# Performance work log

Measured on AMD Instinct MI355X. Metric: run time of the kernel, lower is better.

The kernel has to match this reference:

```python
import jax, jax.numpy as jnp
import numpy as np

B, NBANDS, NCHAN, NTIME = 32, 9, 64, 4096
M = 32
C = M * NBANDS          # 288 spectral-spatial channels
SF = 4                  # strideFactor
TLEN = 2 * SF - 1       # 7 overlapping temporal windows
E = 2                   # embed_dim
H = 2                   # num_heads (head_dim = 1)
NCLASS = 4
BN_EPS = 1e-5


def _renorm(w, maxnorm):
    # torch.renorm(p=2, dim=0): clamp L2 norm of each dim-0 slice to maxnorm
    norms = jnp.sqrt(jnp.sum(w.reshape(w.shape[0], -1) ** 2, axis=1))
    scale = jnp.minimum(1.0, maxnorm / jnp.maximum(norms, 1e-7))
    return w * scale.reshape((-1,) + (1,) * (w.ndim - 1))


def _pos_embed():
    # get_1d_sincos_pos_embed_from_grid(embed_dim=2, len=7)
    pos = np.arange(TLEN, dtype=np.float32)
    omega = 1.0 / (10000.0 ** (np.arange(E // 2, dtype=np.float32) / (E / 2.0)))
    out = pos[:, None] * omega[None, :]
    return jnp.asarray(np.concatenate([np.sin(out), np.cos(out)], axis=1), jnp.float32)  # [TLEN, E]


def setup_inputs() -> dict:
    key = jax.random.key(0)
    ks = jax.random.split(key, 10)
    s = 0.1
    return {
        "x": jax.random.uniform(ks[0], (B, NBANDS, NCHAN, NTIME), jnp.float32),
        "conv_w": jax.random.normal(ks[1], (C, 1, NCHAN, 1), jnp.float32) * s,
        "conv_b": jax.random.normal(ks[2], (C,), jnp.float32) * s,
        "bn_gamma": jnp.ones((C,), jnp.float32),
        "bn_beta": jnp.zeros((C,), jnp.float32),
        "bn_mean": jnp.zeros((C,), jnp.float32),
        "bn_var": jnp.ones((C,), jnp.float32),
        "in_proj_w": jax.random.normal(ks[3], (C, 3 * E, E), jnp.float32) * s,
        "in_proj_b": jax.random.normal(ks[4], (C, 3 * E), jnp.float32) * s,
        "out_proj_w": jax.random.normal(ks[5], (C, E, E), jnp.float32) * s,
        "out_proj_b": jax.random.normal(ks[6], (C, E), jnp.float32) * s,
        "last_w": jax.random.normal(ks[7], (NCLASS, C * TLEN * E), jnp.float32) * s,
        "last_b": jax.random.normal(ks[8], (NCLASS,), jnp.float32) * s,
    }


def _forward(x, conv_w, conv_b, bn_gamma, bn_beta, bn_mean, bn_var,
             in_proj_w, in_proj_b, out_proj_w, out_proj_b, last_w, last_b):
    # --- SCB: grouped conv (nChan,1) + BatchNorm(eval) + swish ---
    w = _renorm(conv_w, 2.0)
    y = jax.lax.conv_general_dilated(
        x, w, window_strides=(1, 1), padding='VALID',
        dimension_numbers=('NCHW', 'OIHW', 'NCHW'),
        feature_group_count=NBANDS) + conv_b[None, :, None, None]      # [B,C,1,NTIME]
    y = (y - bn_mean[None, :, None, None]) * jax.lax.rsqrt(bn_var + BN_EPS)[None, :, None, None]
    y = y * bn_gamma[None, :, None, None] + bn_beta[None, :, None, None]
    y = y * jax.nn.sigmoid(y)  # swish

    # --- overlapping temporal windows stacked on dim 2 ---
    ts = NTIME // (SF * 2)
    xs = jnp.concatenate([y[:, :, :, i * ts:(i + 2) * ts] for i in range(TLEN)], axis=2)  # [B,C,TLEN,2ts]

    # --- tempo_layer: log-var, RMS/mean shape factor ---
    var = jnp.log(jnp.clip(jnp.var(xs, axis=3, keepdims=True, ddof=1), 1e-6, 1e6))
    mean_ = jnp.mean(xs, axis=3, keepdims=True)
    x_rms = jnp.sqrt(jnp.mean(xs ** 2, axis=3, keepdims=True))
    feat = jnp.concatenate([var, x_rms / mean_], axis=3)               # [B,C,TLEN,E]

    # --- batched per-channel multihead self-attention (replaces C-way loop) ---
    yq = feat + _pos_embed()[None, None]                               # [B,C,T,E]
    qkv = jnp.einsum('bcte,cfe->bctf', yq, in_proj_w) + in_proj_b[None, :, None, :]
    q, k, v = jnp.split(qkv, 3, axis=3)
    hd = E // H
    q = q.reshape(B, C, TLEN, H, hd)
    k = k.reshape(B, C, TLEN, H, hd)
    v = v.reshape(B, C, TLEN, H, hd)
    scores = jnp.einsum('bcthd,bcshd->bchts', q, k) / jnp.sqrt(jnp.float32(hd))
    att = jax.nn.softmax(scores, axis=-1)
    o = jnp.einsum('bchts,bcshd->bcthd', att, v).reshape(B, C, TLEN, E)
    o = jnp.einsum('bcte,cfe->bctf', o, out_proj_w) + out_proj_b[None, :, None, :]

    # --- classifier with weight-norm constraint + log-softmax ---
    flat = o.reshape(B, C * TLEN * E)
    lw = _renorm(last_w, 0.5)
    logits = flat @ lw.T + last_b
    return jax.nn.log_softmax(logits, axis=1)


def reference(x, conv_w, conv_b, bn_gamma, bn_beta, bn_mean, bn_var,
              in_proj_w, in_proj_b, out_proj_w, out_proj_b, last_w, last_b):
    return _forward(x, conv_w, conv_b, bn_gamma, bn_beta, bn_mean, bn_var,
                    in_proj_w, in_proj_b, out_proj_w, out_proj_b, last_w, last_b)
```

## Files before the change

### kernel.cpp

```cpp
#include <hip/hip_runtime.h>
#include <math.h>

#define BB     32
#define NBANDS 9
#define NCHAN  64
#define NTIME  4096
#define CC     288
#define TLEN   7
#define NSEG   8
#define SEGLEN 512
#define NCLASS 4

#define WS_WF    0
#define WS_BIAS  (WS_WF + CC*NCHAN)
#define WS_S1    (WS_BIAS + CC)
#define WS_S2    (WS_S1 + BB*CC*NSEG)
#define WS_FLAT  (WS_S2 + BB*CC*NSEG)
#define WS_TOTAL (WS_FLAT + BB*CC*TLEN*2)

__global__ __launch_bounds__(64) void k0_fold(
    const float* __restrict__ cw, const float* __restrict__ cb,
    const float* __restrict__ gam, const float* __restrict__ bet,
    const float* __restrict__ mu, const float* __restrict__ var,
    float* __restrict__ Wf, float* __restrict__ biasf) {
  int c = blockIdx.x;
  int h = threadIdx.x;
  float w = cw[c * NCHAN + h];
  float sq = w * w;
#pragma unroll
  for (int off = 32; off; off >>= 1) sq += __shfl_down(sq, off, 64);
  sq = __shfl(sq, 0, 64);
  float norm = sqrtf(sq);
  float scale = fminf(1.0f, 2.0f / fmaxf(norm, 1e-7f));
  float bns = gam[c] / sqrtf(var[c] + 1e-5f);
  Wf[c * NCHAN + h] = w * scale * bns;
  if (h == 0) biasf[c] = (cb[c] - mu[c]) * bns + bet[c];
}

__global__ __launch_bounds__(256, 4) void k1_conv(
    const float* __restrict__ x, const float* __restrict__ Wf,
    const float* __restrict__ biasf,
    float* __restrict__ S1, float* __restrict__ S2) {
  int gid = blockIdx.x;
  int seg = gid & 7;
  int g = (gid >> 3) % NBANDS;
  int b = gid / (NBANDS * NSEG);
  int tid = threadIdx.x;
  const float* xp = x + (size_t)(b * NBANDS + g) * NCHAN * NTIME + seg * SEGLEN;
  const float* wbase = Wf + g * 32 * NCHAN;
  const float* bbase = biasf + g * 32;

  float acc0[32], acc1[32];
#pragma unroll
  for (int c = 0; c < 32; ++c) { acc0[c] = 0.0f; acc1[c] = 0.0f; }

#pragma unroll 1
  for (int ht = 0; ht < NCHAN; ht += 8) {
    float2 xv[8];
#pragma unroll
    for (int j = 0; j < 8; ++j)
      xv[j] = ((const float2*)(xp + (size_t)(ht + j) * NTIME))[tid];
#pragma unroll
    for (int c = 0; c < 32; ++c) {
#pragma unroll
      for (int j = 0; j < 8; ++j) {
        float w = wbase[c * NCHAN + ht + j];
        acc0[c] = fmaf(w, xv[j].x, acc0[c]);
        acc1[c] = fmaf(w, xv[j].y, acc1[c]);
      }
    }
  }

  __shared__ float part[32][4][2];
  int wave = tid >> 6;
  int lane = tid & 63;

#pragma unroll
  for (int c = 0; c < 32; ++c) {
    float bias = bbase[c];
    float da = acc0[c] + bias;
    float db = acc1[c] + bias;
    float ya = da * __builtin_amdgcn_rcpf(1.0f + __expf(-da));
    float yb = db * __builtin_amdgcn_rcpf(1.0f + __expf(-db));
    float s1 = ya + yb;
    float s2 = fmaf(ya, ya, yb * yb);
#pragma unroll
    for (int off = 32; off; off >>= 1) {
      s1 += __shfl_down(s1, off, 64);
      s2 += __shfl_down(s2, off, 64);
    }
    if (lane == 0) { part[c][wave][0] = s1; part[c][wave][1] = s2; }
  }
  __syncthreads();
  if (tid < 64) {
    int c = tid >> 1;
    int which = tid & 1;
    float v = part[c][0][which] + part[c][1][which] +
              part[c][2][which] + part[c][3][which];
    size_t o = (size_t)((b * CC) + g * 32 + c) * NSEG + seg;
    if (which == 0) S1[o] = v; else S2[o] = v;
  }
}

__global__ __launch_bounds__(256) void k2_attn(
    const float* __restrict__ S1, const float* __restrict__ S2,
    const float* __restrict__ ipw, const float* __restrict__ ipb,
    const float* __restrict__ opw, const float* __restrict__ opb,
    float* __restrict__ flat) {
  const float PSIN[TLEN] = {0.0f, 0.8414709848f, 0.9092974268f, 0.1411200081f,
                            -0.7568024953f, -0.9589242747f, -0.2794154982f};
  const float PCOS[TLEN] = {1.0f, 0.5403023059f, -0.4161468365f, -0.9899924966f,
                            -0.6536436209f, 0.2836621855f, 0.9601702867f};
  int idx = blockIdx.x * blockDim.x + threadIdx.x;
  if (idx >= BB * CC) return;
  int b = idx / CC, c = idx % CC;
  const float* s1 = S1 + (size_t)(b * CC + c) * NSEG;
  const float* s2 = S2 + (size_t)(b * CC + c) * NSEG;

  float yq[TLEN][2];
#pragma unroll
  for (int t = 0; t < TLEN; ++t) {
    float S1w = s1[t] + s1[t + 1];
    float S2w = s2[t] + s2[t + 1];
    float mean = S1w * (1.0f / 1024.0f);
    float var = (S2w - S1w * S1w * (1.0f / 1024.0f)) * (1.0f / 1023.0f);
    var = fminf(fmaxf(var, 1e-6f), 1e6f);
    float rms = sqrtf(S2w * (1.0f / 1024.0f));
    yq[t][0] = __logf(var) + PSIN[t];
    yq[t][1] = rms / mean + PCOS[t];
  }

  const float* W = ipw + c * 12;
  const float* Bp = ipb + c * 6;
  float q[TLEN][2], k[TLEN][2], v[TLEN][2];
#pragma unroll
  for (int t = 0; t < TLEN; ++t) {
#pragma unroll
    for (int f = 0; f < 6; ++f) {
      float val = W[f * 2 + 0] * yq[t][0] + W[f * 2 + 1] * yq[t][1] + Bp[f];
      if (f < 2) q[t][f] = val;
      else if (f < 4) k[t][f - 2] = val;
      else v[t][f - 4] = val;
    }
  }

  float o[TLEN][2];
#pragma unroll
  for (int h = 0; h < 2; ++h) {
#pragma unroll
    for (int t = 0; t < TLEN; ++t) {
      float sc[TLEN];
      float m = -1e30f;
#pragma unroll
      for (int s = 0; s < TLEN; ++s) {
        sc[s] = q[t][h] * k[s][h];
        m = fmaxf(m, sc[s]);
      }
      float sum = 0.0f, acc = 0.0f;
#pragma unroll
      for (int s = 0; s < TLEN; ++s) {
        float e = __expf(sc[s] - m);
        sum += e;
        acc += e * v[s][h];
      }
      o[t][h] = acc / sum;
    }
  }

  const float* Wo = opw + c * 4;
  const float* Bo = opb + c * 2;
  float* out = flat + (size_t)b * (CC * TLEN * 2) + c * (TLEN * 2);
#pragma unroll
  for (int t = 0; t < TLEN; ++t) {
    out[t * 2 + 0] = Wo[0] * o[t][0] + Wo[1] * o[t][1] + Bo[0];
    out[t * 2 + 1] = Wo[2] * o[t][0] + Wo[3] * o[t][1] + Bo[1];
  }
}

__global__ __launch_bounds__(256) void k3_cls(
    const float* __restrict__ flat, const float* __restrict__ lw,
    const float* __restrict__ lb, float* __restrict__ out) {
  const int FEAT = CC * TLEN * 2;
  int b = blockIdx.x;
  int tid = threadIdx.x;
  const float* f = flat + (size_t)b * FEAT;
  float d[NCLASS] = {0, 0, 0, 0}, n2[NCLASS] = {0, 0, 0, 0};
  for (int j = tid; j < FEAT; j += 256) {
    float fv = f[j];
#pragma unroll
    for (int n = 0; n < NCLASS; ++n) {
      float w = lw[n * FEAT + j];
      d[n] = fmaf(fv, w, d[n]);
      n2[n] = fmaf(w, w, n2[n]);
    }
  }
  __shared__ float red[4][8];
  int lane = tid & 63, wave = tid >> 6;
#pragma unroll
  for (int n = 0; n < NCLASS; ++n) {
#pragma unroll
    for (int off = 32; off; off >>= 1) {
      d[n] += __shfl_down(d[n], off, 64);
      n2[n] += __shfl_down(n2[n], off, 64);
    }
  }
  if (lane == 0) {
#pragma unroll
    for (int n = 0; n < NCLASS; ++n) {
      red[wave][n] = d[n];
      red[wave][n + 4] = n2[n];
    }
  }
  __syncthreads();
  if (tid == 0) {
    float logit[NCLASS];
#pragma unroll
    for (int n = 0; n < NCLASS; ++n) {
      float dn = red[0][n] + red[1][n] + red[2][n] + red[3][n];
      float nn = red[0][n + 4] + red[1][n + 4] + red[2][n + 4] + red[3][n + 4];
      float norm = sqrtf(nn);
      float scale = fminf(1.0f, 0.5f / fmaxf(norm, 1e-7f));
      logit[n] = dn * scale + lb[n];
    }
    float m = fmaxf(fmaxf(logit[0], logit[1]), fmaxf(logit[2], logit[3]));
    float s = 0.0f;
#pragma unroll
    for (int n = 0; n < NCLASS; ++n) s += expf(logit[n] - m);
    float ls = logf(s);
#pragma unroll
    for (int n = 0; n < NCLASS; ++n) out[b * NCLASS + n] = logit[n] - m - ls;
  }
}

extern "C" void kernel_launch(void* const* d_in, const int* in_sizes, int n_in,
                              void* d_out, int out_size, void* d_ws, size_t ws_size,
                              hipStream_t stream) {
  const float* x     = (const float*)d_in[0];
  const float* cw    = (const float*)d_in[1];
  const float* cb    = (const float*)d_in[2];
  const float* gam   = (const float*)d_in[3];
  const float* bet   = (const float*)d_in[4];
  const float* mu    = (const float*)d_in[5];
  const float* var   = (const float*)d_in[6];
  const float* ipw   = (const float*)d_in[7];
  const float* ipb   = (const float*)d_in[8];
  const float* opw   = (const float*)d_in[9];
  const float* opb   = (const float*)d_in[10];
  const float* lw    = (const float*)d_in[11];
  const float* lb    = (const float*)d_in[12];
  float* out = (float*)d_out;

  float* ws = (float*)d_ws;
  float* Wf    = ws + WS_WF;
  float* biasf = ws + WS_BIAS;
  float* S1    = ws + WS_S1;
  float* S2    = ws + WS_S2;
  float* flat  = ws + WS_FLAT;

  k0_fold<<<CC, 64, 0, stream>>>(cw, cb, gam, bet, mu, var, Wf, biasf);
  k1_conv<<<BB * NBANDS * NSEG, 256, 0, stream>>>(x, Wf, biasf, S1, S2);
  k2_attn<<<(BB * CC + 255) / 256, 256, 0, stream>>>(S1, S2, ipw, ipb, opw, opb, flat);
  k3_cls<<<BB, 256, 0, stream>>>(flat, lw, lb, out);
}
```

Before: 455.6 us.

## Run grouped spatial conv on MFMA with split-fp16 hi/lo emulation

```diff
diff --git a/kernel.cpp b/kernel.cpp
--- a/kernel.cpp
+++ b/kernel.cpp
@@ -16,15 +16,19 @@
 #define WS_S1    (WS_BIAS + CC)
 #define WS_S2    (WS_S1 + BB*CC*NSEG)
 #define WS_FLAT  (WS_S2 + BB*CC*NSEG)
-#define WS_TOTAL (WS_FLAT + BB*CC*TLEN*2)
+
+typedef _Float16 f16;
+typedef __attribute__((ext_vector_type(8))) _Float16 f16x8;
+typedef __attribute__((ext_vector_type(4))) float floatx4;
 
 __global__ __launch_bounds__(64) void k0_fold(
     const float* __restrict__ cw, const float* __restrict__ cb,
     const float* __restrict__ gam, const float* __restrict__ bet,
     const float* __restrict__ mu, const float* __restrict__ var,
-    float* __restrict__ Wf, float* __restrict__ biasf) {
+    f16* __restrict__ Wh, f16* __restrict__ Wl, float* __restrict__ biasf) {
   int c = blockIdx.x;
   int h = threadIdx.x;
+  int g = c >> 5, cc = c & 31;
   float w = cw[c * NCHAN + h];
   float sq = w * w;
 #pragma unroll
@@ -33,70 +37,128 @@
   float norm = sqrtf(sq);
   float scale = fminf(1.0f, 2.0f / fmaxf(norm, 1e-7f));
   float bns = gam[c] / sqrtf(var[c] + 1e-5f);
-  Wf[c * NCHAN + h] = w * scale * bns;
+  float wf = w * scale * bns;
+  f16 hi = (f16)wf;
+  f16 lo = (f16)(wf - (float)hi);
+  int o = g * (NCHAN * 32) + h * 32 + cc;
+  Wh[o] = hi;
+  Wl[o] = lo;
   if (h == 0) biasf[c] = (cb[c] - mu[c]) * bns + bet[c];
 }
 
-__global__ __launch_bounds__(256, 4) void k1_conv(
-    const float* __restrict__ x, const float* __restrict__ Wf,
-    const float* __restrict__ biasf,
+__global__ __launch_bounds__(256, 2) void k1_conv(
+    const float* __restrict__ x, const f16* __restrict__ Wh,
+    const f16* __restrict__ Wl, const float* __restrict__ biasf,
     float* __restrict__ S1, float* __restrict__ S2) {
   int gid = blockIdx.x;
   int seg = gid & 7;
   int g = (gid >> 3) % NBANDS;
   int b = gid / (NBANDS * NSEG);
   int tid = threadIdx.x;
-  const float* xp = x + (size_t)(b * NBANDS + g) * NCHAN * NTIME + seg * SEGLEN;
-  const float* wbase = Wf + g * 32 * NCHAN;
-  const float* bbase = biasf + g * 32;
-
-  float acc0[32], acc1[32];
-#pragma unroll
-  for (int c = 0; c < 32; ++c) { acc0[c] = 0.0f; acc1[c] = 0.0f; }
+  int wave = tid >> 6, lane = tid & 63;
+  int quad = lane >> 4, li = lane & 15;
+
+  const float* xp = x + (size_t)(b * NBANDS + g) * NCHAN * NTIME;
+  const f16* wh = Wh + g * (NCHAN * 32);
+  const f16* wl = Wl + g * (NCHAN * 32);
+
+  f16x8 ah[2][2], al[2][2];
+#pragma unroll
+  for (int mt = 0; mt < 2; ++mt)
+#pragma unroll
+    for (int kb = 0; kb < 2; ++kb)
+#pragma unroll
+      for (int j = 0; j < 8; ++j) {
+        int idx = (kb * 32 + quad * 8 + j) * 32 + mt * 16 + li;
+        ah[mt][kb][j] = wh[idx];
+        al[mt][kb][j] = wl[idx];
+      }
+
+  float biasr[2][4];
+#pragma unroll
+  for (int mt = 0; mt < 2; ++mt)
+#pragma unroll
+    for (int r = 0; r < 4; ++r)
+      biasr[mt][r] = biasf[g * 32 + mt * 16 + quad * 4 + r];
+
+  float s1a[2][4], s2a[2][4];
+#pragma unroll
+  for (int mt = 0; mt < 2; ++mt)
+#pragma unroll
+    for (int r = 0; r < 4; ++r) { s1a[mt][r] = 0.0f; s2a[mt][r] = 0.0f; }
 
 #pragma unroll 1
-  for (int ht = 0; ht < NCHAN; ht += 8) {
-    float2 xv[8];
-#pragma unroll
-    for (int j = 0; j < 8; ++j)
-      xv[j] = ((const float2*)(xp + (size_t)(ht + j) * NTIME))[tid];
-#pragma unroll
-    for (int c = 0; c < 32; ++c) {
-#pragma unroll
-      for (int j = 0; j < 8; ++j) {
-        float w = wbase[c * NCHAN + ht + j];
-        acc0[c] = fmaf(w, xv[j].x, acc0[c]);
-        acc1[c] = fmaf(w, xv[j].y, acc1[c]);
-      }
-    }
-  }
-
-  __shared__ float part[32][4][2];
-  int wave = tid >> 6;
-  int lane = tid & 63;
-
-#pragma unroll
-  for (int c = 0; c < 32; ++c) {
-    float bias = bbase[c];
-    float da = acc0[c] + bias;
-    float db = acc1[c] + bias;
-    float ya = da * __builtin_amdgcn_rcpf(1.0f + __expf(-da));
-    float yb = db * __builtin_amdgcn_rcpf(1.0f + __expf(-db));
-    float s1 = ya + yb;
-    float s2 = fmaf(ya, ya, yb * yb);
-#pragma unroll
-    for (int off = 32; off; off >>= 1) {
-      s1 += __shfl_down(s1, off, 64);
-      s2 += __shfl_down(s2, off, 64);
-    }
-    if (lane == 0) { part[c][wave][0] = s1; part[c][wave][1] = s2; }
+  for (int ch = 0; ch < 2; ++ch) {
+    int tc = seg * SEGLEN + wave * 128 + ch * 64;
+    float4 v4[2][8];
+#pragma unroll
+    for (int kb = 0; kb < 2; ++kb)
+#pragma unroll
+      for (int j = 0; j < 8; ++j)
+        v4[kb][j] = *(const float4*)(xp + (size_t)(kb * 32 + quad * 8 + j) * NTIME
+                                     + tc + li * 4);
+#pragma unroll
+    for (int tau = 0; tau < 4; ++tau) {
+      f16x8 bh[2], bl[2];
+#pragma unroll
+      for (int kb = 0; kb < 2; ++kb)
+#pragma unroll
+        for (int j = 0; j < 8; ++j) {
+          float v = ((const float*)&v4[kb][j])[tau];
+          f16 hi = (f16)v;
+          bh[kb][j] = hi;
+          bl[kb][j] = (f16)(v - (float)hi);
+        }
+      floatx4 acc0 = {0.0f, 0.0f, 0.0f, 0.0f};
+      floatx4 acc1 = {0.0f, 0.0f, 0.0f, 0.0f};
+#pragma unroll
+      for (int kb = 0; kb < 2; ++kb) {
+        acc0 = __builtin_amdgcn_mfma_f32_16x16x32_f16(ah[0][kb], bh[kb], acc0, 0, 0, 0);
+        acc0 = __builtin_amdgcn_mfma_f32_16x16x32_f16(ah[0][kb], bl[kb], acc0, 0, 0, 0);
+        acc0 = __builtin_amdgcn_mfma_f32_16x16x32_f16(al[0][kb], bh[kb], acc0, 0, 0, 0);
+        acc1 = __builtin_amdgcn_mfma_f32_16x16x32_f16(ah[1][kb], bh[kb], acc1, 0, 0, 0);
+        acc1 = __builtin_amdgcn_mfma_f32_16x16x32_f16(ah[1][kb], bl[kb], acc1, 0, 0, 0);
+        acc1 = __builtin_amdgcn_mfma_f32_16x16x32_f16(al[1][kb], bh[kb], acc1, 0, 0, 0);
+      }
+#pragma unroll
+      for (int r = 0; r < 4; ++r) {
+        float d0 = acc0[r] + biasr[0][r];
+        float d1 = acc1[r] + biasr[1][r];
+        float y0 = d0 * __builtin_amdgcn_rcpf(1.0f + __expf(-d0));
+        float y1 = d1 * __builtin_amdgcn_rcpf(1.0f + __expf(-d1));
+        s1a[0][r] += y0; s2a[0][r] = fmaf(y0, y0, s2a[0][r]);
+        s1a[1][r] += y1; s2a[1][r] = fmaf(y1, y1, s2a[1][r]);
+      }
+    }
+  }
+
+#pragma unroll
+  for (int off = 8; off; off >>= 1) {
+#pragma unroll
+    for (int mt = 0; mt < 2; ++mt)
+#pragma unroll
+      for (int r = 0; r < 4; ++r) {
+        s1a[mt][r] += __shfl_down(s1a[mt][r], off, 16);
+        s2a[mt][r] += __shfl_down(s2a[mt][r], off, 16);
+      }
+  }
+
+  __shared__ float part[2][32][4];
+  if (li == 0) {
+#pragma unroll
+    for (int mt = 0; mt < 2; ++mt)
+#pragma unroll
+      for (int r = 0; r < 4; ++r) {
+        int c = mt * 16 + quad * 4 + r;
+        part[0][c][wave] = s1a[mt][r];
+        part[1][c][wave] = s2a[mt][r];
+      }
   }
   __syncthreads();
   if (tid < 64) {
-    int c = tid >> 1;
-    int which = tid & 1;
-    float v = part[c][0][which] + part[c][1][which] +
-              part[c][2][which] + part[c][3][which];
+    int c = tid >> 1, which = tid & 1;
+    float v = part[which][c][0] + part[which][c][1] +
+              part[which][c][2] + part[which][c][3];
     size_t o = (size_t)((b * CC) + g * 32 + c) * NSEG + seg;
     if (which == 0) S1[o] = v; else S2[o] = v;
   }
@@ -251,14 +313,15 @@
   float* out = (float*)d_out;
 
   float* ws = (float*)d_ws;
-  float* Wf    = ws + WS_WF;
+  f16* Wh = (f16*)(ws + WS_WF);
+  f16* Wl = Wh + CC * NCHAN;
   float* biasf = ws + WS_BIAS;
   float* S1    = ws + WS_S1;
   float* S2    = ws + WS_S2;
   float* flat  = ws + WS_FLAT;
 
-  k0_fold<<<CC, 64, 0, stream>>>(cw, cb, gam, bet, mu, var, Wf, biasf);
-  k1_conv<<<BB * NBANDS * NSEG, 256, 0, stream>>>(x, Wf, biasf, S1, S2);
+  k0_fold<<<CC, 64, 0, stream>>>(cw, cb, gam, bet, mu, var, Wh, Wl, biasf);
+  k1_conv<<<BB * NBANDS * NSEG, 256, 0, stream>>>(x, Wh, Wl, biasf, S1, S2);
   k2_attn<<<(BB * CC + 255) / 256, 256, 0, stream>>>(S1, S2, ipw, ipb, opw, opb, flat);
   k3_cls<<<BB, 256, 0, stream>>>(flat, lw, lb, out);
 }
```

After: 437.8 us. -3.9%, faster.
